# Kernel tuning notes

Hardware: AMD Instinct MI355X
Metric: run time of the kernel (lower is better)

Reference implementation:

```python
import jax, jax.numpy as jnp
import numpy as np

NUM_EXPERTS = 8
TOP_K = 2
N_TOKENS = 4096
HIDDEN = 1024
EXPERT_DIM = 4096


def setup_inputs() -> dict:
    key = jax.random.key(0)
    ks = jax.random.split(key, 4)
    x = jax.random.normal(ks[0], (N_TOKENS, HIDDEN), dtype=jnp.float32)
    Wg = jax.random.normal(ks[1], (HIDDEN, NUM_EXPERTS), dtype=jnp.float32) * 0.02
    bg = jnp.zeros((NUM_EXPERTS,), dtype=jnp.float32)
    W1 = jax.random.normal(ks[2], (NUM_EXPERTS, HIDDEN, EXPERT_DIM), dtype=jnp.float32) * 0.02
    b1 = jnp.zeros((NUM_EXPERTS, EXPERT_DIM), dtype=jnp.float32)
    W2 = jax.random.normal(ks[3], (NUM_EXPERTS, EXPERT_DIM, HIDDEN), dtype=jnp.float32) * 0.02
    b2 = jnp.zeros((NUM_EXPERTS, HIDDEN), dtype=jnp.float32)
    return {"x": x, "Wg": Wg, "bg": bg, "W1": W1, "b1": b1, "W2": W2, "b2": b2}


def reference(x, Wg, bg, W1, b1, W2, b2):
    # Gating: softmax over experts, then top-k routing with renormalized gates.
    gate_probs = jax.nn.softmax(x @ Wg + bg, axis=-1)          # [N, E]
    top_gates, top_idx = jax.lax.top_k(gate_probs, TOP_K)      # [N, K]
    top_gates = top_gates / jnp.sum(top_gates, axis=-1, keepdims=True)
    # Per-(token, expert) combine weight: sum of gates routed to that expert.
    combine = jnp.sum(
        jax.nn.one_hot(top_idx, NUM_EXPERTS, dtype=x.dtype) * top_gates[..., None],
        axis=1,
    )  # [N, E]
    # Expert MLPs: Linear -> ReLU -> Linear (dropout=0 at eval, norm=False).
    out = jnp.zeros_like(x)
    for e in range(NUM_EXPERTS):
        h = jax.nn.relu(x @ W1[e] + b1[e])                      # [N, expert_dim]
        y = h @ W2[e] + b2[e]                                   # [N, hidden]
        out = out + combine[:, e:e + 1] * y
    # Switch-style auxiliary load-balancing loss.
    expert_counts = jnp.sum(gate_probs, axis=0)                 # [E]
    expert_fractions = expert_counts / jnp.sum(expert_counts)
    gate_means = jnp.mean(gate_probs, axis=0)
    aux_loss = NUM_EXPERTS * jnp.sum(expert_fractions * gate_means)
    return out, aux_loss
```

## Files before the change

kernel.cpp:

```cpp
#include <hip/hip_runtime.h>


typedef unsigned short u16;
typedef __bf16 bf16x8 __attribute__((ext_vector_type(8)));
typedef float  f32x4  __attribute__((ext_vector_type(4)));

#define NTOK 4096
#define HID  1024
#define EDIM 4096
#define NEXP 8
#define MAXMT 72

__device__ __forceinline__ u16 f32_bf16(float f) {
  unsigned int u = __float_as_uint(f);
  u += 0x7FFFu + ((u >> 16) & 1u);
  return (u16)(u >> 16);
}

__global__ void gate_kernel(const float* __restrict__ x,
                            const float* __restrict__ Wg,
                            const float* __restrict__ bg,
                            float* __restrict__ combine,
                            float* __restrict__ counts,
                            int* __restrict__ icnt,
                            int* __restrict__ top2idx,
                            float* __restrict__ top2g) {
  __shared__ float lc[NEXP];
  int t = threadIdx.x;
  if (t < NEXP) lc[t] = 0.f;
  __syncthreads();
  int token = blockIdx.x * 4 + (t >> 6);
  int lane = t & 63;
  float s[NEXP] = {};
  const float* xr = x + (size_t)token * HID;
  for (int h = lane; h < HID; h += 64) {
    float xv = xr[h];
    const float* wrow = Wg + (size_t)h * NEXP;
#pragma unroll
    for (int e = 0; e < NEXP; ++e) s[e] += xv * wrow[e];
  }
#pragma unroll
  for (int off = 32; off > 0; off >>= 1) {
#pragma unroll
    for (int e = 0; e < NEXP; ++e) s[e] += __shfl_xor(s[e], off);
  }
  float m = -1e30f;
#pragma unroll
  for (int e = 0; e < NEXP; ++e) { s[e] += bg[e]; m = fmaxf(m, s[e]); }
  float p[NEXP]; float sum = 0.f;
#pragma unroll
  for (int e = 0; e < NEXP; ++e) { p[e] = expf(s[e] - m); sum += p[e]; }
  float inv = 1.f / sum;
#pragma unroll
  for (int e = 0; e < NEXP; ++e) p[e] *= inv;
  int i1 = 0; float g1 = p[0];
#pragma unroll
  for (int e = 1; e < NEXP; ++e) if (p[e] > g1) { g1 = p[e]; i1 = e; }
  int i2 = -1; float g2 = -1.f;
#pragma unroll
  for (int e = 0; e < NEXP; ++e) if (e != i1 && p[e] > g2) { g2 = p[e]; i2 = e; }
  float ginv = 1.f / (g1 + g2);
  if (lane == 0) {
#pragma unroll
    for (int e = 0; e < NEXP; ++e) {
      float c = (e == i1) ? g1 * ginv : (e == i2) ? g2 * ginv : 0.f;
      combine[(size_t)token * NEXP + e] = c;
      atomicAdd(&lc[e], p[e]);
    }
    top2idx[token * 2] = i1; top2idx[token * 2 + 1] = i2;
    top2g[token * 2] = g1 * ginv; top2g[token * 2 + 1] = g2 * ginv;
    atomicAdd(&icnt[i1], 1); atomicAdd(&icnt[i2], 1);
  }
  __syncthreads();
  if (t < NEXP) atomicAdd(&counts[t], lc[t]);
}

__global__ void aux_kernel(const float* __restrict__ counts, float* __restrict__ aux_out) {
  float s = 0.f;
#pragma unroll
  for (int e = 0; e < NEXP; ++e) s += counts[e];
  float a = 0.f;
#pragma unroll
  for (int e = 0; e < NEXP; ++e) a += (counts[e] / s) * (counts[e] / (float)NTOK);
  aux_out[0] = (float)NEXP * a;
}

__global__ void off_kernel(const int* __restrict__ icnt, int* __restrict__ ioff,
                           int* __restrict__ cursor, int* __restrict__ nmtP,
                           int* __restrict__ mtE, int* __restrict__ mtRow0,
                           int* __restrict__ mtValid) {
  int s = 0;
  int loc[NEXP];
  for (int e = 0; e < NEXP; ++e) { loc[e] = s; ioff[e] = s; s += icnt[e]; cursor[e] = 0; }
  int nm = 0;
  for (int e = 0; e < NEXP; ++e) {
    int c = icnt[e];
    int tiles = (c + 127) >> 7;
    for (int mt = 0; mt < tiles; ++mt) {
      mtE[nm] = e; mtRow0[nm] = loc[e] + (mt << 7);
      int v = c - (mt << 7); mtValid[nm] = v > 128 ? 128 : v;
      nm++;
    }
  }
  nmtP[0] = nm;
}

__global__ void fill_kernel(const int* __restrict__ top2idx, const int* __restrict__ ioff,
                            int* __restrict__ cursor, int* __restrict__ tok) {
  int i = blockIdx.x * 256 + threadIdx.x;
  if (i >= NTOK * 2) return;
  int t = i >> 1, k = i & 1;
  int e = top2idx[i];
  int pos = atomicAdd(&cursor[e], 1);
  tok[ioff[e] + pos] = t | (k << 16);
}

__global__ void cvt_kernel(const float* __restrict__ in, u16* __restrict__ out) {
  size_t i = ((size_t)blockIdx.x * 256 + threadIdx.x) * 4;
  float4 v = *(const float4*)(in + i);
  ushort4 o = make_ushort4(f32_bf16(v.x), f32_bf16(v.y), f32_bf16(v.z), f32_bf16(v.w));
  *(ushort4*)(out + i) = o;
}

__global__ void cvtT_kernel(const float* __restrict__ W, u16* __restrict__ WT, int R, int C) {
  __shared__ float tile[32][33];
  int tx = threadIdx.x, ty = threadIdx.y;
  size_t eoff = (size_t)blockIdx.z * R * C;
  const float* Wp = W + eoff;
  u16* WTp = WT + eoff;
  int c0 = blockIdx.x * 32, r0 = blockIdx.y * 32;
#pragma unroll
  for (int i = 0; i < 4; ++i)
    tile[ty + i * 8][tx] = Wp[(size_t)(r0 + ty + i * 8) * C + c0 + tx];
  __syncthreads();
#pragma unroll
  for (int i = 0; i < 4; ++i)
    WTp[(size_t)(c0 + ty + i * 8) * R + r0 + tx] = f32_bf16(tile[tx][ty + i * 8]);
}

template<int MODE>
__global__ __launch_bounds__(256) void gemm_sparse(
    const u16* __restrict__ A, const u16* __restrict__ Wt,
    const int* __restrict__ nmtP, const int* __restrict__ mtE,
    const int* __restrict__ mtRow0, const int* __restrict__ mtValid,
    const int* __restrict__ tok,
    const float* __restrict__ bias, u16* __restrict__ Hout, float* __restrict__ Ypair)
{
  constexpr int KDIM = (MODE == 1) ? HID : EDIM;
  constexpr int NDIM = (MODE == 1) ? EDIM : HID;
  constexpr int NT = NDIM / 128;

  int item = blockIdx.x;
  if (item >= nmtP[0] * NT) return;
  int gmt = item / NT;
  int nt = item - gmt * NT;
  int e = mtE[gmt], row0 = mtRow0[gmt], valid = mtValid[gmt];

  __shared__ __align__(16) u16 As[128 * 32];
  __shared__ __align__(16) u16 Bs[128 * 32];
  const int t = threadIdx.x;
  const int lane = t & 63;
  const int w = t >> 6;
  const int wr = w >> 1, wc = w & 1;
  const int bn0 = nt << 7;
  const int kq = lane >> 4;
  const int r  = lane & 15;

  const u16* Bb = Wt + ((size_t)e * NDIM + bn0) * KDIM;

  size_t arow[2];
#pragma unroll
  for (int c = 0; c < 2; ++c) {
    int idx = c * 256 + t;
    int row = idx >> 2;
    if (MODE == 1) {
      int rr = (row < valid) ? row : 0;
      arow[c] = (size_t)(tok[row0 + rr] & 0xFFFF) * KDIM;
    } else {
      arow[c] = (size_t)(row0 + row) * KDIM;
    }
  }

  f32x4 acc[4][4] = {};

  for (int k0 = 0; k0 < KDIM; k0 += 32) {
    __syncthreads();
#pragma unroll
    for (int c = 0; c < 2; ++c) {
      int idx = c * 256 + t;
      int row = idx >> 2;
      int kc  = (idx & 3) << 3;
      __builtin_amdgcn_global_load_lds(
          (__attribute__((address_space(1))) void*)(A + arow[c] + k0 + kc),
          (__attribute__((address_space(3))) void*)(As + idx * 8), 16, 0, 0);
      __builtin_amdgcn_global_load_lds(
          (__attribute__((address_space(1))) void*)(Bb + (size_t)row * KDIM + k0 + kc),
          (__attribute__((address_space(3))) void*)(Bs + idx * 8), 16, 0, 0);
    }
    __syncthreads();

    bf16x8 af[4], bfr[4];
#pragma unroll
    for (int f = 0; f < 4; ++f) {
      af[f]  = *(const bf16x8*)(As + (wr * 64 + f * 16 + r) * 32 + kq * 8);
      bfr[f] = *(const bf16x8*)(Bs + (wc * 64 + f * 16 + r) * 32 + kq * 8);
    }
#pragma unroll
    for (int fm = 0; fm < 4; ++fm) {
#pragma unroll
      for (int fn = 0; fn < 4; ++fn) {
        acc[fm][fn] = __builtin_amdgcn_mfma_f32_16x16x32_bf16(af[fm], bfr[fn], acc[fm][fn], 0, 0, 0);
      }
    }
  }

  if (MODE == 1) {
#pragma unroll
    for (int fn = 0; fn < 4; ++fn) {
      int col = bn0 + wc * 64 + fn * 16 + r;
      float bv = bias[e * EDIM + col];
#pragma unroll
      for (int fm = 0; fm < 4; ++fm) {
#pragma unroll
        for (int j = 0; j < 4; ++j) {
          int lr = wr * 64 + fm * 16 + kq * 4 + j;
          if (lr < valid) {
            float v = acc[fm][fn][j] + bv;
            v = v > 0.f ? v : 0.f;
            Hout[(size_t)(row0 + lr) * EDIM + col] = f32_bf16(v);
          }
        }
      }
    }
  } else {
#pragma unroll
    for (int fm = 0; fm < 4; ++fm) {
#pragma unroll
      for (int j = 0; j < 4; ++j) {
        int lr = wr * 64 + fm * 16 + kq * 4 + j;
        if (lr < valid) {
          int entry = tok[row0 + lr];
          int tt = entry & 0xFFFF, ss = entry >> 16;
          float* yrow = Ypair + ((size_t)ss * NTOK + tt) * HID;
#pragma unroll
          for (int fn = 0; fn < 4; ++fn) {
            int col = bn0 + wc * 64 + fn * 16 + r;
            yrow[col] = acc[fm][fn][j] + bias[e * HID + col];
          }
        }
      }
    }
  }
}

__global__ void final_kernel(const float* __restrict__ top2g,
                             const float* __restrict__ Ypair,
                             float* __restrict__ out) {
  size_t idx4 = (size_t)blockIdx.x * 256 + threadIdx.x;
  size_t base = idx4 * 4;
  int t = (int)(base >> 10);
  float g0 = top2g[t * 2], g1 = top2g[t * 2 + 1];
  float4 y0 = *(const float4*)(Ypair + base);
  float4 y1 = *(const float4*)(Ypair + (size_t)NTOK * HID + base);
  float4 o;
  o.x = g0 * y0.x + g1 * y1.x;
  o.y = g0 * y0.y + g1 * y1.y;
  o.z = g0 * y0.z + g1 * y1.z;
  o.w = g0 * y0.w + g1 * y1.w;
  *(float4*)(out + base) = o;
}

__global__ void init_out_kernel(const float* __restrict__ combine,
                                const float* __restrict__ b2,
                                float* __restrict__ out) {
  size_t idx = (size_t)blockIdx.x * 256 + threadIdx.x;
  int i = (int)(idx >> 10), j = (int)(idx & 1023);
  float v = 0.f;
#pragma unroll
  for (int e = 0; e < NEXP; ++e) v += combine[(size_t)i * NEXP + e] * b2[e * HID + j];
  out[idx] = v;
}

template<int MODE>
__global__ __launch_bounds__(256) void gemm_kernel(
    const u16* __restrict__ A, const u16* __restrict__ BT,
    int M, int N, int K,
    const float* __restrict__ bias, u16* __restrict__ Hout,
    const float* __restrict__ combine, int expert, float* __restrict__ Out)
{
  __shared__ __align__(16) u16 As[128 * 32];
  __shared__ __align__(16) u16 Bs[128 * 32];
  const int t = threadIdx.x;
  const int lane = t & 63;
  const int w = t >> 6;
  const int wr = w >> 1, wc = w & 1;
  const int nbn = N >> 7;
  const int bm0 = (int)(blockIdx.x / nbn) << 7;
  const int bn0 = (int)(blockIdx.x % nbn) << 7;
  const int kq = lane >> 4;
  const int r  = lane & 15;
  f32x4 acc[4][4] = {};
  const u16* Ab = A + (size_t)bm0 * K;
  const u16* Bb = BT + (size_t)bn0 * K;
  for (int k0 = 0; k0 < K; k0 += 32) {
    __syncthreads();
#pragma unroll
    for (int c = 0; c < 2; ++c) {
      int idx = c * 256 + t;
      int row = idx >> 2;
      int kc  = (idx & 3) << 3;
      __builtin_amdgcn_global_load_lds(
          (__attribute__((address_space(1))) void*)(Ab + (size_t)row * K + k0 + kc),
          (__attribute__((address_space(3))) void*)(As + idx * 8), 16, 0, 0);
      __builtin_amdgcn_global_load_lds(
          (__attribute__((address_space(1))) void*)(Bb + (size_t)row * K + k0 + kc),
          (__attribute__((address_space(3))) void*)(Bs + idx * 8), 16, 0, 0);
    }
    __syncthreads();
    bf16x8 af[4], bfr[4];
#pragma unroll
    for (int f = 0; f < 4; ++f) {
      af[f]  = *(const bf16x8*)(As + (wr * 64 + f * 16 + r) * 32 + kq * 8);
      bfr[f] = *(const bf16x8*)(Bs + (wc * 64 + f * 16 + r) * 32 + kq * 8);
    }
#pragma unroll
    for (int fm = 0; fm < 4; ++fm) {
#pragma unroll
      for (int fn = 0; fn < 4; ++fn) {
        acc[fm][fn] = __builtin_amdgcn_mfma_f32_16x16x32_bf16(af[fm], bfr[fn], acc[fm][fn], 0, 0, 0);
      }
    }
  }
  if (MODE == 1) {
#pragma unroll
    for (int fn = 0; fn < 4; ++fn) {
      int col = bn0 + wc * 64 + fn * 16 + r;
      float bv = bias[col];
#pragma unroll
      for (int fm = 0; fm < 4; ++fm) {
#pragma unroll
        for (int j = 0; j < 4; ++j) {
          int row = bm0 + wr * 64 + fm * 16 + kq * 4 + j;
          float v = acc[fm][fn][j] + bv;
          v = v > 0.f ? v : 0.f;
          Hout[(size_t)row * N + col] = f32_bf16(v);
        }
      }
    }
  } else {
#pragma unroll
    for (int fm = 0; fm < 4; ++fm) {
      float cg[4];
#pragma unroll
      for (int j = 0; j < 4; ++j) {
        int row = bm0 + wr * 64 + fm * 16 + kq * 4 + j;
        cg[j] = combine[(size_t)row * NEXP + expert];
      }
#pragma unroll
      for (int fn = 0; fn < 4; ++fn) {
        int col = bn0 + wc * 64 + fn * 16 + r;
#pragma unroll
        for (int j = 0; j < 4; ++j) {
          int row = bm0 + wr * 64 + fm * 16 + kq * 4 + j;
          Out[(size_t)row * N + col] += cg[j] * acc[fm][fn][j];
        }
      }
    }
  }
}

extern "C" void kernel_launch(void* const* d_in, const int* in_sizes, int n_in,
                              void* d_out, int out_size, void* d_ws, size_t ws_size,
                              hipStream_t stream) {
  (void)in_sizes; (void)n_in; (void)out_size;
  const float* x  = (const float*)d_in[0];
  const float* Wg = (const float*)d_in[1];
  const float* bg = (const float*)d_in[2];
  const float* W1 = (const float*)d_in[3];
  const float* b1 = (const float*)d_in[4];
  const float* W2 = (const float*)d_in[5];
  const float* b2 = (const float*)d_in[6];
  float* out = (float*)d_out;

  char* ws = (char*)d_ws;
  float* counts  = (float*)(ws);
  int*   icnt    = (int*)(ws + 64);
  int*   ioff    = (int*)(ws + 128);
  int*   cursor  = (int*)(ws + 192);
  int*   nmtP    = (int*)(ws + 256);
  int*   mtE     = (int*)(ws + 512);
  int*   mtRow0  = (int*)(ws + 1024);
  int*   mtValid = (int*)(ws + 1536);
  int*   top2idx = (int*)(ws + 4096);
  float* top2g   = (float*)(ws + 36864);
  int*   tok     = (int*)(ws + 69632);
  float* combine = (float*)(ws + 131072);

  const size_t MB = 1024 * 1024;
  u16* xbf = (u16*)(ws + 1 * MB);

  const size_t REQ = 241 * MB;
  bool sparse = ws_size >= REQ;

  hipMemsetAsync(ws, 0, 1024, stream);
  gate_kernel<<<NTOK / 4, 256, 0, stream>>>(x, Wg, bg, combine, counts, icnt, top2idx, top2g);
  aux_kernel<<<1, 1, 0, stream>>>(counts, out + (size_t)NTOK * HID);
  cvt_kernel<<<(NTOK * HID) / 1024, 256, 0, stream>>>(x, xbf);

  if (sparse) {
    u16* w1tA  = (u16*)(ws + 9 * MB);
    u16* w2tA  = (u16*)(ws + 73 * MB);
    u16* H     = (u16*)(ws + 137 * MB);
    float* Ypair = (float*)(ws + 209 * MB);

    cvtT_kernel<<<dim3(EDIM / 32, HID / 32, NEXP), dim3(32, 8), 0, stream>>>(W1, w1tA, HID, EDIM);
    cvtT_kernel<<<dim3(HID / 32, EDIM / 32, NEXP), dim3(32, 8), 0, stream>>>(W2, w2tA, EDIM, HID);
    off_kernel<<<1, 1, 0, stream>>>(icnt, ioff, cursor, nmtP, mtE, mtRow0, mtValid);
    fill_kernel<<<(NTOK * 2 + 255) / 256, 256, 0, stream>>>(top2idx, ioff, cursor, tok);

    gemm_sparse<1><<<MAXMT * (EDIM / 128), 256, 0, stream>>>(
        xbf, w1tA, nmtP, mtE, mtRow0, mtValid, tok, b1, H, nullptr);
    gemm_sparse<2><<<MAXMT * (HID / 128), 256, 0, stream>>>(
        H, w2tA, nmtP, mtE, mtRow0, mtValid, tok, b2, nullptr, Ypair);
    final_kernel<<<(NTOK * HID / 4) / 256, 256, 0, stream>>>(top2g, Ypair, out);
  } else {
    u16* w1t = (u16*)(ws + 9 * MB);
    u16* w2t = (u16*)(ws + 17 * MB);
    u16* H   = (u16*)(ws + 25 * MB);
    init_out_kernel<<<(NTOK * HID) / 256, 256, 0, stream>>>(combine, b2, out);
    for (int e = 0; e < NEXP; ++e) {
      cvtT_kernel<<<dim3(EDIM / 32, HID / 32, 1), dim3(32, 8), 0, stream>>>(
          W1 + (size_t)e * HID * EDIM, w1t, HID, EDIM);
      gemm_kernel<1><<<(NTOK / 128) * (EDIM / 128), 256, 0, stream>>>(
          xbf, w1t, NTOK, EDIM, HID, b1 + (size_t)e * EDIM, H, nullptr, 0, nullptr);
      cvtT_kernel<<<dim3(HID / 32, EDIM / 32, 1), dim3(32, 8), 0, stream>>>(
          W2 + (size_t)e * EDIM * HID, w2t, EDIM, HID);
      gemm_kernel<2><<<(NTOK / 128) * (HID / 128), 256, 0, stream>>>(
          H, w2t, NTOK, HID, EDIM, nullptr, nullptr, combine, e, out);
    }
  }
}
```

Before: 504.9 us.

## Double-buffer LDS in sparse expert GEMM and vectorize epilogue stores

```diff
diff --git a/kernel.cpp b/kernel.cpp
--- a/kernel.cpp
+++ b/kernel.cpp
@@ -149,6 +149,7 @@
   constexpr int KDIM = (MODE == 1) ? HID : EDIM;
   constexpr int NDIM = (MODE == 1) ? EDIM : HID;
   constexpr int NT = NDIM / 128;
+  constexpr int NK = KDIM / 32;
 
   int item = blockIdx.x;
   if (item >= nmtP[0] * NT) return;
@@ -156,8 +157,8 @@
   int nt = item - gmt * NT;
   int e = mtE[gmt], row0 = mtRow0[gmt], valid = mtValid[gmt];
 
-  __shared__ __align__(16) u16 As[128 * 32];
-  __shared__ __align__(16) u16 Bs[128 * 32];
+  __shared__ __align__(16) u16 As[2][128 * 32];
+  __shared__ __align__(16) u16 Bs[2][128 * 32];
   const int t = threadIdx.x;
   const int lane = t & 63;
   const int w = t >> 6;
@@ -169,10 +170,12 @@
   const u16* Bb = Wt + ((size_t)e * NDIM + bn0) * KDIM;
 
   size_t arow[2];
+  int srow[2];
 #pragma unroll
   for (int c = 0; c < 2; ++c) {
     int idx = c * 256 + t;
     int row = idx >> 2;
+    srow[c] = row;
     if (MODE == 1) {
       int rr = (row < valid) ? row : 0;
       arow[c] = (size_t)(tok[row0 + rr] & 0xFFFF) * KDIM;
@@ -181,72 +184,81 @@
     }
   }
 
-  f32x4 acc[4][4] = {};
-
-  for (int k0 = 0; k0 < KDIM; k0 += 32) {
-    __syncthreads();
+  auto stage = [&](int buf, int k0) {
 #pragma unroll
     for (int c = 0; c < 2; ++c) {
       int idx = c * 256 + t;
-      int row = idx >> 2;
       int kc  = (idx & 3) << 3;
       __builtin_amdgcn_global_load_lds(
-          (__attribute__((address_space(1))) void*)(A + arow[c] + k0 + kc),
-          (__attribute__((address_space(3))) void*)(As + idx * 8), 16, 0, 0);
+          (const __attribute__((address_space(1))) void*)(A + arow[c] + k0 + kc),
+          (__attribute__((address_space(3))) void*)(&As[buf][idx * 8]), 16, 0, 0);
       __builtin_amdgcn_global_load_lds(
-          (__attribute__((address_space(1))) void*)(Bb + (size_t)row * KDIM + k0 + kc),
-          (__attribute__((address_space(3))) void*)(Bs + idx * 8), 16, 0, 0);
+          (const __attribute__((address_space(1))) void*)(Bb + (size_t)srow[c] * KDIM + k0 + kc),
+          (__attribute__((address_space(3))) void*)(&Bs[buf][idx * 8]), 16, 0, 0);
+    }
+  };
+
+  f32x4 acc[4][4] = {};
+
+  stage(0, 0);
+  __syncthreads();
+  int cur = 0;
+  for (int ks = 0; ks < NK; ++ks) {
+    if (ks + 1 < NK) stage(cur ^ 1, (ks + 1) * 32);
+    bf16x8 af[4], bfr[4];
+#pragma unroll
+    for (int f = 0; f < 4; ++f) {
+      af[f]  = *(const bf16x8*)(&As[cur][(wr * 64 + f * 16 + r) * 32 + kq * 8]);
+      bfr[f] = *(const bf16x8*)(&Bs[cur][(wc * 64 + f * 16 + r) * 32 + kq * 8]);
+    }
+#pragma unroll
+    for (int fm = 0; fm < 4; ++fm) {
+#pragma unroll
+      for (int fn = 0; fn < 4; ++fn) {
+        acc[fn][fm] = __builtin_amdgcn_mfma_f32_16x16x32_bf16(bfr[fn], af[fm], acc[fn][fm], 0, 0, 0);
+      }
     }
     __syncthreads();
-
-    bf16x8 af[4], bfr[4];
-#pragma unroll
-    for (int f = 0; f < 4; ++f) {
-      af[f]  = *(const bf16x8*)(As + (wr * 64 + f * 16 + r) * 32 + kq * 8);
-      bfr[f] = *(const bf16x8*)(Bs + (wc * 64 + f * 16 + r) * 32 + kq * 8);
-    }
+    cur ^= 1;
+  }
+
+  if (MODE == 1) {
 #pragma unroll
     for (int fm = 0; fm < 4; ++fm) {
-#pragma unroll
-      for (int fn = 0; fn < 4; ++fn) {
-        acc[fm][fn] = __builtin_amdgcn_mfma_f32_16x16x32_bf16(af[fm], bfr[fn], acc[fm][fn], 0, 0, 0);
-      }
-    }
-  }
-
-  if (MODE == 1) {
-#pragma unroll
-    for (int fn = 0; fn < 4; ++fn) {
-      int col = bn0 + wc * 64 + fn * 16 + r;
-      float bv = bias[e * EDIM + col];
-#pragma unroll
-      for (int fm = 0; fm < 4; ++fm) {
-#pragma unroll
-        for (int j = 0; j < 4; ++j) {
-          int lr = wr * 64 + fm * 16 + kq * 4 + j;
-          if (lr < valid) {
-            float v = acc[fm][fn][j] + bv;
-            v = v > 0.f ? v : 0.f;
-            Hout[(size_t)(row0 + lr) * EDIM + col] = f32_bf16(v);
-          }
+      int lr = wr * 64 + fm * 16 + r;
+      if (lr < valid) {
+        u16* hrow = Hout + (size_t)(row0 + lr) * EDIM;
+#pragma unroll
+        for (int fn = 0; fn < 4; ++fn) {
+          int col0 = bn0 + wc * 64 + fn * 16 + kq * 4;
+          float4 bv = *(const float4*)(bias + (size_t)e * EDIM + col0);
+          float v0 = acc[fn][fm][0] + bv.x; v0 = v0 > 0.f ? v0 : 0.f;
+          float v1 = acc[fn][fm][1] + bv.y; v1 = v1 > 0.f ? v1 : 0.f;
+          float v2 = acc[fn][fm][2] + bv.z; v2 = v2 > 0.f ? v2 : 0.f;
+          float v3 = acc[fn][fm][3] + bv.w; v3 = v3 > 0.f ? v3 : 0.f;
+          ushort4 h = make_ushort4(f32_bf16(v0), f32_bf16(v1), f32_bf16(v2), f32_bf16(v3));
+          *(ushort4*)(hrow + col0) = h;
         }
       }
     }
   } else {
 #pragma unroll
     for (int fm = 0; fm < 4; ++fm) {
-#pragma unroll
-      for (int j = 0; j < 4; ++j) {
-        int lr = wr * 64 + fm * 16 + kq * 4 + j;
-        if (lr < valid) {
-          int entry = tok[row0 + lr];
-          int tt = entry & 0xFFFF, ss = entry >> 16;
-          float* yrow = Ypair + ((size_t)ss * NTOK + tt) * HID;
-#pragma unroll
-          for (int fn = 0; fn < 4; ++fn) {
-            int col = bn0 + wc * 64 + fn * 16 + r;
-            yrow[col] = acc[fm][fn][j] + bias[e * HID + col];
-          }
+      int lr = wr * 64 + fm * 16 + r;
+      if (lr < valid) {
+        int entry = tok[row0 + lr];
+        int tt = entry & 0xFFFF, ss = entry >> 16;
+        float* yrow = Ypair + ((size_t)ss * NTOK + tt) * HID;
+#pragma unroll
+        for (int fn = 0; fn < 4; ++fn) {
+          int col0 = bn0 + wc * 64 + fn * 16 + kq * 4;
+          float4 bv = *(const float4*)(bias + (size_t)e * HID + col0);
+          float4 o;
+          o.x = acc[fn][fm][0] + bv.x;
+          o.y = acc[fn][fm][1] + bv.y;
+          o.z = acc[fn][fm][2] + bv.z;
+          o.w = acc[fn][fm][3] + bv.w;
+          *(float4*)(yrow + col0) = o;
         }
       }
     }
@@ -310,10 +322,10 @@
       int row = idx >> 2;
       int kc  = (idx & 3) << 3;
       __builtin_amdgcn_global_load_lds(
-          (__attribute__((address_space(1))) void*)(Ab + (size_t)row * K + k0 + kc),
+          (const __attribute__((address_space(1))) void*)(Ab + (size_t)row * K + k0 + kc),
           (__attribute__((address_space(3))) void*)(As + idx * 8), 16, 0, 0);
       __builtin_amdgcn_global_load_lds(
-          (__attribute__((address_space(1))) void*)(Bb + (size_t)row * K + k0 + kc),
+          (const __attribute__((address_space(1))) void*)(Bb + (size_t)row * K + k0 + kc),
           (__attribute__((address_space(3))) void*)(Bs + idx * 8), 16, 0, 0);
     }
     __syncthreads();
```

After: 519.4 us. 1.03x slower.
